# Performance work log

Hardware: AMD Instinct MI355X
Metric: run time of the kernel (lower is better)

Reference implementation:

```python
import jax, jax.numpy as jnp
import numpy as np
from jax import lax


def _l2norm(x):
    # normalize rows: x / ||x||_2, matching torch vector_norm along dim=-1
    return x / jnp.linalg.norm(x, axis=-1, keepdims=True)


def setup_inputs() -> dict:
    key = jax.random.key(0)
    k1, k2, k3, k4, k5 = jax.random.split(key, 5)
    B, N, Ds, Dd = 64, 20000, 4096, 2048
    return {
        "f_content": jax.random.normal(k1, (B, Ds), dtype=jnp.float32),
        "f_distorsion": jax.random.normal(k2, (B, Dd), dtype=jnp.float32),
        "semantic_db": jax.random.normal(k3, (N, Ds), dtype=jnp.float32),
        "distorsion_db": jax.random.normal(k4, (N, Dd), dtype=jnp.float32),
        "metrics": jax.random.uniform(k5, (N,), dtype=jnp.float32),
        "K": 9,
    }


def reference(f_content, f_distorsion, semantic_db, distorsion_db, metrics, K):
    # L2-normalize query features and DB features (DB is normalized at init in torch)
    fc = _l2norm(f_content)            # [B, Ds]
    fd = _l2norm(f_distorsion)         # [B, Dd]
    sem_db = _l2norm(semantic_db)      # [N, Ds]
    dst_db = _l2norm(distorsion_db)    # [N, Dd]

    # full cosine similarity matmuls, then descending top-K (== sort desc + slice K)
    sem_cos = fc @ sem_db.T            # [B, N]
    dst_cos = fd @ dst_db.T            # [B, N]
    _, idx_sem = lax.top_k(sem_cos, K)   # [B, K]
    _, idx_dst = lax.top_k(dst_cos, K)   # [B, K]

    # gather metric values for retrieved neighbors; interleave sem/dst per m
    m_sem = metrics[idx_sem]           # [B, K]
    m_dst = metrics[idx_dst]           # [B, K]
    retrieved = jnp.stack([m_sem, m_dst], axis=-1).reshape(m_sem.shape[0], 2 * K)  # [B, 2K]
    result = retrieved.mean(axis=-1)   # [B]
    return result, retrieved
```

## Files before the change

### kernel.cpp

```cpp
#include <hip/hip_runtime.h>
#include <math.h>


typedef _Float16 half8 __attribute__((ext_vector_type(8)));
typedef float    f32x4 __attribute__((ext_vector_type(4)));

#define NDB   20000
#define NQ    64
#define KSEM  4096
#define KDST  2048
#define KC    2048
#define NSTEP (KC / 64)
#define BN    64
#define NTILE 313
#define K2    16
#define SEG   8
#define SEGSZ (NDB / SEG)

__device__ __forceinline__ void async_cp16(const void* g, void* l) {
    __builtin_amdgcn_global_load_lds(
        (const __attribute__((address_space(1))) void*)g,
        (__attribute__((address_space(3))) void*)l, 16, 0, 0);
}

__global__ __launch_bounds__(256) void qsplit_kernel(
    const float* __restrict__ fc, const float* __restrict__ fd,
    _Float16* __restrict__ apack_sem, _Float16* __restrict__ apack_dst)
{
    const int idx = (int)blockIdx.x * 256 + (int)threadIdx.x;
    const int NSEM8 = NQ * KSEM / 8;
    const float* src; _Float16* dst; int row, g8, K;
    if (idx < NSEM8) { src = fc; dst = apack_sem; K = KSEM; row = idx >> 9; g8 = idx & 511; }
    else { const int j = idx - NSEM8; src = fd; dst = apack_dst; K = KDST; row = j >> 8; g8 = j & 255; }

    const float* p = src + (size_t)row * K + g8 * 8;
    const float4 v0 = ((const float4*)p)[0];
    const float4 v1 = ((const float4*)p)[1];
    const float xs[8] = {v0.x, v0.y, v0.z, v0.w, v1.x, v1.y, v1.z, v1.w};
    half8 hi, lo;
    #pragma unroll
    for (int e = 0; e < 8; ++e) {
        const _Float16 h = (_Float16)xs[e];
        hi[e] = h;
        lo[e] = (_Float16)((xs[e] - (float)h) * 4096.0f);
    }
    const int sec = g8 >> 2, kg = g8 & 3;
    const int u = (row << 2) + (((row >> 1) & 3) ^ kg);
    half8* d8 = (half8*)dst;
    d8[sec * 512 + u]       = hi;
    d8[sec * 512 + 256 + u] = lo;
}

__global__ __launch_bounds__(256, 2) void score_kernel(
    const float* __restrict__ sdb, const float* __restrict__ ddb,
    const _Float16* __restrict__ apack_sem, const _Float16* __restrict__ apack_dst,
    float* __restrict__ semp0, float* __restrict__ semp1, float* __restrict__ dstp,
    float* __restrict__ nsq0, float* __restrict__ nsq1, float* __restrict__ nsqd)
{
    __shared__ __align__(16) _Float16 A_lds[2][8192];
    __shared__ __align__(16) float    B_lds[2][4096];

    const int tid  = threadIdx.x;
    const int lane = tid & 63, w = tid >> 6;
    const int bid  = (int)blockIdx.x;
    const int mkc  = bid / NTILE;
    const int nt   = bid % NTILE;
    const int n0   = nt * BN;

    const float* D; const _Float16* AP; float *SOUT, *NOUT; int Ks, koff;
    if (mkc == 0)      { D=sdb; AP=apack_sem; SOUT=semp0; NOUT=nsq0; Ks=KSEM; koff=0;  }
    else if (mkc == 1) { D=sdb; AP=apack_sem; SOUT=semp1; NOUT=nsq1; Ks=KSEM; koff=KC; }
    else               { D=ddb; AP=apack_dst; SOUT=dstp;  NOUT=nsqd; Ks=KDST; koff=0;  }

    const int u0 = w * 128 + lane,      r0 = u0 >> 3, c0 = (u0 & 7) ^ (r0 & 7);
    const int u1 = u0 + 64,             r1 = u1 >> 3, c1 = (u1 & 7) ^ (r1 & 7);
    const int rg0 = (n0 + r0 < NDB) ? n0 + r0 : NDB - 1;
    const int rg1 = (n0 + r1 < NDB) ? n0 + r1 : NDB - 1;
    const float* gB0 = D + (size_t)rg0 * Ks + koff + c0 * 4;
    const float* gB1 = D + (size_t)rg1 * Ks + koff + c1 * 4;
    const uint4* gA = (const uint4*)AP + ((size_t)koff >> 5) * 512 + w * 64 + lane;

    const int lr = lane & 15, kg = lane >> 4;
    const int qh = w >> 1, nh = w & 1;
    const int rowA0 = qh * 32 + lr;
    const int rowA1 = rowA0 + 16;
    const int uA0 = ((rowA0 << 2) + (((rowA0 >> 1) & 3) ^ kg)) * 8;
    const int uA1 = ((rowA1 << 2) + (((rowA1 >> 1) & 3) ^ kg)) * 8;
    const int rB0 = nh * 32 + lr;
    const int rB1 = rB0 + 16;
    const int oB00 = rB0 * 32 + (((kg * 2 + 0) ^ (rB0 & 7)) << 2);
    const int oB01 = rB0 * 32 + (((kg * 2 + 1) ^ (rB0 & 7)) << 2);
    const int oB10 = rB1 * 32 + (((kg * 2 + 0) ^ (rB1 & 7)) << 2);
    const int oB11 = rB1 * 32 + (((kg * 2 + 1) ^ (rB1 & 7)) << 2);

    f32x4 acc_h[2][2], acc_x[2][2];
    const f32x4 zz = {0.f, 0.f, 0.f, 0.f};
    #pragma unroll
    for (int i = 0; i < 2; ++i)
        #pragma unroll
        for (int j = 0; j < 2; ++j) { acc_h[i][j] = zz; acc_x[i][j] = zz; }
    float sq0 = 0.f, sq1 = 0.f;

    auto STAGE = [&](int s, int buf) {
        #pragma unroll
        for (int sec = 0; sec < 2; ++sec) {
            const size_t gsec = (size_t)(2 * s + sec);
            async_cp16(gA + gsec * 512,       &A_lds[buf][sec * 4096 + w * 512]);
            async_cp16(gA + gsec * 512 + 256, &A_lds[buf][sec * 4096 + 2048 + w * 512]);
            async_cp16(gB0 + gsec * 32, &B_lds[buf][sec * 2048 + w * 512]);
            async_cp16(gB1 + gsec * 32, &B_lds[buf][sec * 2048 + w * 512 + 256]);
        }
    };

    auto COMPUTE = [&](int buf) {
        #pragma unroll
        for (int sec = 0; sec < 2; ++sec) {
            const float*    Bb = &B_lds[buf][sec * 2048];
            const _Float16* Ab = &A_lds[buf][sec * 4096];
            half8 bh0, bl0, bh1, bl1;
            {
                const f32x4 p = *(const f32x4*)(Bb + oB00);
                const f32x4 q = *(const f32x4*)(Bb + oB01);
                const float xs[8] = {p[0], p[1], p[2], p[3], q[0], q[1], q[2], q[3]};
                #pragma unroll
                for (int e = 0; e < 8; ++e) {
                    const float x = xs[e];
                    sq0 = fmaf(x, x, sq0);
                    const _Float16 h = (_Float16)x;
                    bh0[e] = h;
                    bl0[e] = (_Float16)((x - (float)h) * 4096.0f);
                }
            }
            {
                const f32x4 p = *(const f32x4*)(Bb + oB10);
                const f32x4 q = *(const f32x4*)(Bb + oB11);
                const float xs[8] = {p[0], p[1], p[2], p[3], q[0], q[1], q[2], q[3]};
                #pragma unroll
                for (int e = 0; e < 8; ++e) {
                    const float x = xs[e];
                    sq1 = fmaf(x, x, sq1);
                    const _Float16 h = (_Float16)x;
                    bh1[e] = h;
                    bl1[e] = (_Float16)((x - (float)h) * 4096.0f);
                }
            }
            const half8 ah0 = *(const half8*)(Ab + uA0);
            const half8 av0 = *(const half8*)(Ab + 2048 + uA0);
            const half8 ah1 = *(const half8*)(Ab + uA1);
            const half8 av1 = *(const half8*)(Ab + 2048 + uA1);

            acc_h[0][0] = __builtin_amdgcn_mfma_f32_16x16x32_f16(ah0, bh0, acc_h[0][0], 0, 0, 0);
            acc_x[0][0] = __builtin_amdgcn_mfma_f32_16x16x32_f16(ah0, bl0, acc_x[0][0], 0, 0, 0);
            acc_x[0][0] = __builtin_amdgcn_mfma_f32_16x16x32_f16(av0, bh0, acc_x[0][0], 0, 0, 0);
            acc_h[0][1] = __builtin_amdgcn_mfma_f32_16x16x32_f16(ah0, bh1, acc_h[0][1], 0, 0, 0);
            acc_x[0][1] = __builtin_amdgcn_mfma_f32_16x16x32_f16(ah0, bl1, acc_x[0][1], 0, 0, 0);
            acc_x[0][1] = __builtin_amdgcn_mfma_f32_16x16x32_f16(av0, bh1, acc_x[0][1], 0, 0, 0);
            acc_h[1][0] = __builtin_amdgcn_mfma_f32_16x16x32_f16(ah1, bh0, acc_h[1][0], 0, 0, 0);
            acc_x[1][0] = __builtin_amdgcn_mfma_f32_16x16x32_f16(ah1, bl0, acc_x[1][0], 0, 0, 0);
            acc_x[1][0] = __builtin_amdgcn_mfma_f32_16x16x32_f16(av1, bh0, acc_x[1][0], 0, 0, 0);
            acc_h[1][1] = __builtin_amdgcn_mfma_f32_16x16x32_f16(ah1, bh1, acc_h[1][1], 0, 0, 0);
            acc_x[1][1] = __builtin_amdgcn_mfma_f32_16x16x32_f16(ah1, bl1, acc_x[1][1], 0, 0, 0);
            acc_x[1][1] = __builtin_amdgcn_mfma_f32_16x16x32_f16(av1, bh1, acc_x[1][1], 0, 0, 0);
        }
    };

    STAGE(0, 0); STAGE(1, 1);

    for (int s = 0; s < NSTEP; ++s) {
        if (s < NSTEP - 1) { asm volatile("s_waitcnt vmcnt(8)" ::: "memory"); }
        else               { asm volatile("s_waitcnt vmcnt(0)" ::: "memory"); }
        __builtin_amdgcn_s_barrier();
        COMPUTE(s & 1);
        __builtin_amdgcn_s_barrier();
        if (s + 2 < NSTEP) STAGE(s + 2, s & 1);
    }

    sq0 += __shfl_xor(sq0, 16); sq0 += __shfl_xor(sq0, 32);
    sq1 += __shfl_xor(sq1, 16); sq1 += __shfl_xor(sq1, 32);
    if (qh == 0 && lane < 16) {
        const int nn0 = n0 + nh * 32 + lane;
        const int nn1 = nn0 + 16;
        if (nn0 < NDB) NOUT[nn0] = sq0;
        if (nn1 < NDB) NOUT[nn1] = sq1;
    }

    #pragma unroll
    for (int i = 0; i < 2; ++i)
        #pragma unroll
        for (int j = 0; j < 2; ++j) {
            const int n = n0 + nh * 32 + j * 16 + lr;
            if (n < NDB) {
                #pragma unroll
                for (int rr = 0; rr < 4; ++rr) {
                    const int q = qh * 32 + i * 16 + kg * 4 + rr;
                    SOUT[(size_t)q * NDB + n] = acc_h[i][j][rr] + acc_x[i][j][rr] * (1.0f / 4096.0f);
                }
            }
        }
}

__global__ __launch_bounds__(256) void topk_seg_kernel(
    const float* __restrict__ semp0, const float* __restrict__ semp1,
    const float* __restrict__ dstp,
    const float* __restrict__ nsq0, const float* __restrict__ nsq1,
    const float* __restrict__ nsqd,
    float* __restrict__ cand_val, int* __restrict__ cand_idx)
{
    __shared__ float sv[256][K2];
    __shared__ int   si[256][K2];

    const int tid = threadIdx.x;
    const int mb  = (int)blockIdx.x >> 3;
    const int seg = (int)blockIdx.x & 7;
    const int b = mb & 63;
    const int m = mb >> 6;

    float v[K2]; int ix[K2];
    #pragma unroll
    for (int k = 0; k < K2; ++k) { v[k] = -INFINITY; ix[k] = 0x7fffffff; }

    const size_t roff = (size_t)b * NDB;
    const int iend = (seg + 1) * SEGSZ;
    for (int i = seg * SEGSZ + tid; i < iend; i += 256) {
        float sval;
        if (m == 0) {
            sval = (semp0[roff + i] + semp1[roff + i]) * (1.0f / sqrtf(nsq0[i] + nsq1[i]));
        } else {
            sval = dstp[roff + i] * (1.0f / sqrtf(nsqd[i]));
        }
        if (sval > v[0]) {
            bool bt[K2];
            bt[0] = true;
            #pragma unroll
            for (int j = 1; j < K2; ++j) bt[j] = sval > v[j];
            #pragma unroll
            for (int j = 0; j < K2 - 1; ++j) {
                v[j]  = bt[j+1] ? v[j+1]  : (bt[j] ? sval : v[j]);
                ix[j] = bt[j+1] ? ix[j+1] : (bt[j] ? i    : ix[j]);
            }
            v[K2-1]  = bt[K2-1] ? sval : v[K2-1];
            ix[K2-1] = bt[K2-1] ? i    : ix[K2-1];
        }
    }

    #pragma unroll
    for (int k = 0; k < K2; ++k) { sv[tid][k] = v[k]; si[tid][k] = ix[k]; }
    __syncthreads();

    for (int s2 = 128; s2 >= 1; s2 >>= 1) {
        if (tid < s2) {
            float rv[K2]; int ri[K2];
            int pa = K2 - 1, pb = K2 - 1;
            #pragma unroll
            for (int k = K2 - 1; k >= 0; --k) {
                const float va = sv[tid][pa];      const int ia = si[tid][pa];
                const float vb = sv[tid + s2][pb]; const int ib = si[tid + s2][pb];
                const bool takeA = (va > vb) || (va == vb && ia < ib);
                rv[k] = takeA ? va : vb;
                ri[k] = takeA ? ia : ib;
                if (takeA) --pa; else --pb;
            }
            #pragma unroll
            for (int k = 0; k < K2; ++k) { sv[tid][k] = rv[k]; si[tid][k] = ri[k]; }
        }
        __syncthreads();
    }

    if (tid < K2) {
        cand_val[(size_t)mb * 128 + seg * K2 + tid] = sv[0][K2 - 1 - tid];
        cand_idx[(size_t)mb * 128 + seg * K2 + tid] = si[0][K2 - 1 - tid];
    }
}

__global__ __launch_bounds__(128) void merge_kernel(
    const float* __restrict__ cand_val, const int* __restrict__ cand_idx,
    const float* __restrict__ metrics, float* __restrict__ out_ret)
{
    __shared__ float v[128];
    __shared__ int   id[128];
    const int tid = threadIdx.x;
    const int mb  = (int)blockIdx.x;
    const int b = mb & 63;
    const int m = mb >> 6;
    v[tid]  = cand_val[(size_t)mb * 128 + tid];
    id[tid] = cand_idx[(size_t)mb * 128 + tid];
    __syncthreads();
    const float mv = v[tid];
    const int   mi = id[tid];
    int rank = 0;
    for (int j = 0; j < 128; ++j)
        rank += (v[j] > mv) || (v[j] == mv && id[j] < mi);
    if (rank < 9) out_ret[(size_t)b * 18 + 2 * rank + m] = metrics[mi];
}

__global__ void finalize_kernel(float* __restrict__ d_out)
{
    const int b = threadIdx.x;
    const float* r = d_out + 64 + (size_t)b * 18;
    float s = 0.f;
    #pragma unroll
    for (int j = 0; j < 18; ++j) s += r[j];
    d_out[b] = s * (1.0f / 18.0f);
}

extern "C" void kernel_launch(void* const* d_in, const int* in_sizes, int n_in,
                              void* d_out, int out_size, void* d_ws, size_t ws_size,
                              hipStream_t stream)
{
    const float* fc  = (const float*)d_in[0];
    const float* fd  = (const float*)d_in[1];
    const float* sdb = (const float*)d_in[2];
    const float* ddb = (const float*)d_in[3];
    const float* met = (const float*)d_in[4];

    float* semp0 = (float*)d_ws;
    float* semp1 = semp0 + (size_t)NQ * NDB;
    float* dstp  = semp1 + (size_t)NQ * NDB;
    float* nsq0  = dstp  + (size_t)NQ * NDB;
    float* nsq1  = nsq0 + NDB;
    float* nsqd  = nsq1 + NDB;
    _Float16* apack_sem = (_Float16*)(nsqd + NDB);
    _Float16* apack_dst = apack_sem + (size_t)NQ * KSEM * 2;
    float* cand_val = (float*)(apack_dst + (size_t)NQ * KDST * 2);
    int*   cand_idx = (int*)(cand_val + 128 * 128);

    float* out = (float*)d_out;

    qsplit_kernel<<<dim3(192), dim3(256), 0, stream>>>(fc, fd, apack_sem, apack_dst);
    score_kernel<<<dim3(3 * NTILE), dim3(256), 0, stream>>>(
        sdb, ddb, apack_sem, apack_dst, semp0, semp1, dstp, nsq0, nsq1, nsqd);
    topk_seg_kernel<<<dim3(128 * SEG), dim3(256), 0, stream>>>(
        semp0, semp1, dstp, nsq0, nsq1, nsqd, cand_val, cand_idx);
    merge_kernel<<<dim3(128), dim3(128), 0, stream>>>(cand_val, cand_idx, met, out + 64);
    finalize_kernel<<<dim3(1), dim3(64), 0, stream>>>(out);
}
```

Baseline: 169.6 us.

## Drop query low-part MFMAs and add exact FP32 rerank of top-16 candidates

The query side now keeps only the fp16 high part, which removes one third of the MFMAs and halves the A-tile LDS footprint and loads. Occupancy is raised to 3 blocks per SM. To make up for the lower-precision scores, the merge kernel keeps the top 16 candidates, and a new rerank kernel recomputes their exact fp32 cosine similarity before choosing the top 9. This adds a small extra kernel, and the final answer can be wrong if a true top-9 item falls outside the approximate top-16.

```diff
diff --git a/kernel.cpp b/kernel.cpp
--- a/kernel.cpp
+++ b/kernel.cpp
@@ -37,27 +37,21 @@
     const float4 v0 = ((const float4*)p)[0];
     const float4 v1 = ((const float4*)p)[1];
     const float xs[8] = {v0.x, v0.y, v0.z, v0.w, v1.x, v1.y, v1.z, v1.w};
-    half8 hi, lo;
-    #pragma unroll
-    for (int e = 0; e < 8; ++e) {
-        const _Float16 h = (_Float16)xs[e];
-        hi[e] = h;
-        lo[e] = (_Float16)((xs[e] - (float)h) * 4096.0f);
-    }
+    half8 hi;
+    #pragma unroll
+    for (int e = 0; e < 8; ++e) hi[e] = (_Float16)xs[e];
     const int sec = g8 >> 2, kg = g8 & 3;
     const int u = (row << 2) + (((row >> 1) & 3) ^ kg);
-    half8* d8 = (half8*)dst;
-    d8[sec * 512 + u]       = hi;
-    d8[sec * 512 + 256 + u] = lo;
-}
-
-__global__ __launch_bounds__(256, 2) void score_kernel(
+    ((half8*)dst)[sec * 256 + u] = hi;
+}
+
+__global__ __launch_bounds__(256, 3) void score_kernel(
     const float* __restrict__ sdb, const float* __restrict__ ddb,
     const _Float16* __restrict__ apack_sem, const _Float16* __restrict__ apack_dst,
     float* __restrict__ semp0, float* __restrict__ semp1, float* __restrict__ dstp,
     float* __restrict__ nsq0, float* __restrict__ nsq1, float* __restrict__ nsqd)
 {
-    __shared__ __align__(16) _Float16 A_lds[2][8192];
+    __shared__ __align__(16) _Float16 A_lds[2][4096];
     __shared__ __align__(16) float    B_lds[2][4096];
 
     const int tid  = threadIdx.x;
@@ -78,7 +72,7 @@
     const int rg1 = (n0 + r1 < NDB) ? n0 + r1 : NDB - 1;
     const float* gB0 = D + (size_t)rg0 * Ks + koff + c0 * 4;
     const float* gB1 = D + (size_t)rg1 * Ks + koff + c1 * 4;
-    const uint4* gA = (const uint4*)AP + ((size_t)koff >> 5) * 512 + w * 64 + lane;
+    const uint4* gA = (const uint4*)AP + ((size_t)koff >> 5) * 256 + w * 64 + lane;
 
     const int lr = lane & 15, kg = lane >> 4;
     const int qh = w >> 1, nh = w & 1;
@@ -105,10 +99,9 @@
         #pragma unroll
         for (int sec = 0; sec < 2; ++sec) {
             const size_t gsec = (size_t)(2 * s + sec);
-            async_cp16(gA + gsec * 512,       &A_lds[buf][sec * 4096 + w * 512]);
-            async_cp16(gA + gsec * 512 + 256, &A_lds[buf][sec * 4096 + 2048 + w * 512]);
-            async_cp16(gB0 + gsec * 32, &B_lds[buf][sec * 2048 + w * 512]);
-            async_cp16(gB1 + gsec * 32, &B_lds[buf][sec * 2048 + w * 512 + 256]);
+            async_cp16(gA + gsec * 256,  &A_lds[buf][sec * 2048 + w * 512]);
+            async_cp16(gB0 + gsec * 32,  &B_lds[buf][sec * 2048 + w * 512]);
+            async_cp16(gB1 + gsec * 32,  &B_lds[buf][sec * 2048 + w * 512 + 256]);
         }
     };
 
@@ -116,7 +109,7 @@
         #pragma unroll
         for (int sec = 0; sec < 2; ++sec) {
             const float*    Bb = &B_lds[buf][sec * 2048];
-            const _Float16* Ab = &A_lds[buf][sec * 4096];
+            const _Float16* Ab = &A_lds[buf][sec * 2048];
             half8 bh0, bl0, bh1, bl1;
             {
                 const f32x4 p = *(const f32x4*)(Bb + oB00);
@@ -145,29 +138,23 @@
                 }
             }
             const half8 ah0 = *(const half8*)(Ab + uA0);
-            const half8 av0 = *(const half8*)(Ab + 2048 + uA0);
             const half8 ah1 = *(const half8*)(Ab + uA1);
-            const half8 av1 = *(const half8*)(Ab + 2048 + uA1);
 
             acc_h[0][0] = __builtin_amdgcn_mfma_f32_16x16x32_f16(ah0, bh0, acc_h[0][0], 0, 0, 0);
             acc_x[0][0] = __builtin_amdgcn_mfma_f32_16x16x32_f16(ah0, bl0, acc_x[0][0], 0, 0, 0);
-            acc_x[0][0] = __builtin_amdgcn_mfma_f32_16x16x32_f16(av0, bh0, acc_x[0][0], 0, 0, 0);
             acc_h[0][1] = __builtin_amdgcn_mfma_f32_16x16x32_f16(ah0, bh1, acc_h[0][1], 0, 0, 0);
             acc_x[0][1] = __builtin_amdgcn_mfma_f32_16x16x32_f16(ah0, bl1, acc_x[0][1], 0, 0, 0);
-            acc_x[0][1] = __builtin_amdgcn_mfma_f32_16x16x32_f16(av0, bh1, acc_x[0][1], 0, 0, 0);
             acc_h[1][0] = __builtin_amdgcn_mfma_f32_16x16x32_f16(ah1, bh0, acc_h[1][0], 0, 0, 0);
             acc_x[1][0] = __builtin_amdgcn_mfma_f32_16x16x32_f16(ah1, bl0, acc_x[1][0], 0, 0, 0);
-            acc_x[1][0] = __builtin_amdgcn_mfma_f32_16x16x32_f16(av1, bh0, acc_x[1][0], 0, 0, 0);
             acc_h[1][1] = __builtin_amdgcn_mfma_f32_16x16x32_f16(ah1, bh1, acc_h[1][1], 0, 0, 0);
             acc_x[1][1] = __builtin_amdgcn_mfma_f32_16x16x32_f16(ah1, bl1, acc_x[1][1], 0, 0, 0);
-            acc_x[1][1] = __builtin_amdgcn_mfma_f32_16x16x32_f16(av1, bh1, acc_x[1][1], 0, 0, 0);
         }
     };
 
     STAGE(0, 0); STAGE(1, 1);
 
     for (int s = 0; s < NSTEP; ++s) {
-        if (s < NSTEP - 1) { asm volatile("s_waitcnt vmcnt(8)" ::: "memory"); }
+        if (s < NSTEP - 1) { asm volatile("s_waitcnt vmcnt(6)" ::: "memory"); }
         else               { asm volatile("s_waitcnt vmcnt(0)" ::: "memory"); }
         __builtin_amdgcn_s_barrier();
         COMPUTE(s & 1);
@@ -274,14 +261,12 @@
 
 __global__ __launch_bounds__(128) void merge_kernel(
     const float* __restrict__ cand_val, const int* __restrict__ cand_idx,
-    const float* __restrict__ metrics, float* __restrict__ out_ret)
+    int* __restrict__ idx_ws)
 {
     __shared__ float v[128];
     __shared__ int   id[128];
     const int tid = threadIdx.x;
     const int mb  = (int)blockIdx.x;
-    const int b = mb & 63;
-    const int m = mb >> 6;
     v[tid]  = cand_val[(size_t)mb * 128 + tid];
     id[tid] = cand_idx[(size_t)mb * 128 + tid];
     __syncthreads();
@@ -290,7 +275,63 @@
     int rank = 0;
     for (int j = 0; j < 128; ++j)
         rank += (v[j] > mv) || (v[j] == mv && id[j] < mi);
-    if (rank < 9) out_ret[(size_t)b * 18 + 2 * rank + m] = metrics[mi];
+    if (rank < K2) idx_ws[(size_t)mb * K2 + rank] = mi;
+}
+
+__global__ __launch_bounds__(256) void rerank_kernel(
+    const float* __restrict__ fc, const float* __restrict__ fd,
+    const float* __restrict__ sdb, const float* __restrict__ ddb,
+    const int* __restrict__ idx_ws, const float* __restrict__ metrics,
+    float* __restrict__ out_ret)
+{
+    __shared__ float cosv[K2];
+    __shared__ int   cidx[K2];
+
+    const int tid = threadIdx.x;
+    const int lane = tid & 63, w = tid >> 6;
+    const int bid = (int)blockIdx.x;
+    const int b = bid & 63;
+    const int m = bid >> 6;
+
+    const float* Q  = (m == 0) ? fc + (size_t)b * KSEM : fd + (size_t)b * KDST;
+    const float* DB = (m == 0) ? sdb : ddb;
+    const int Ks = (m == 0) ? KSEM : KDST;
+    const int nf4 = Ks / 4;
+
+    for (int c = w; c < K2; c += 4) {
+        const int idx = idx_ws[(size_t)bid * K2 + c];
+        const float4* Q4 = (const float4*)Q;
+        const float4* R4 = (const float4*)(DB + (size_t)idx * Ks);
+        float dot = 0.f, sq = 0.f;
+        for (int it = lane; it < nf4; it += 64) {
+            const float4 qv = Q4[it];
+            const float4 rv = R4[it];
+            dot = fmaf(qv.x, rv.x, dot); sq = fmaf(rv.x, rv.x, sq);
+            dot = fmaf(qv.y, rv.y, dot); sq = fmaf(rv.y, rv.y, sq);
+            dot = fmaf(qv.z, rv.z, dot); sq = fmaf(rv.z, rv.z, sq);
+            dot = fmaf(qv.w, rv.w, dot); sq = fmaf(rv.w, rv.w, sq);
+        }
+        #pragma unroll
+        for (int off = 1; off < 64; off <<= 1) {
+            dot += __shfl_xor(dot, off);
+            sq  += __shfl_xor(sq,  off);
+        }
+        if (lane == 0) {
+            cosv[c] = dot / sqrtf(sq);
+            cidx[c] = idx;
+        }
+    }
+    __syncthreads();
+
+    if (tid < K2) {
+        const float v = cosv[tid];
+        const int   id = cidx[tid];
+        int rank = 0;
+        #pragma unroll
+        for (int j = 0; j < K2; ++j)
+            rank += (cosv[j] > v) || (cosv[j] == v && cidx[j] < id);
+        if (rank < 9) out_ret[(size_t)b * 18 + 2 * rank + m] = metrics[id];
+    }
 }
 
 __global__ void finalize_kernel(float* __restrict__ d_out)
@@ -320,9 +361,10 @@
     float* nsq1  = nsq0 + NDB;
     float* nsqd  = nsq1 + NDB;
     _Float16* apack_sem = (_Float16*)(nsqd + NDB);
-    _Float16* apack_dst = apack_sem + (size_t)NQ * KSEM * 2;
-    float* cand_val = (float*)(apack_dst + (size_t)NQ * KDST * 2);
+    _Float16* apack_dst = apack_sem + (size_t)NQ * KSEM;
+    float* cand_val = (float*)(apack_dst + (size_t)NQ * KDST);
     int*   cand_idx = (int*)(cand_val + 128 * 128);
+    int*   idx_ws   = cand_idx + 128 * 128;
 
     float* out = (float*)d_out;
 
@@ -331,6 +373,8 @@
         sdb, ddb, apack_sem, apack_dst, semp0, semp1, dstp, nsq0, nsq1, nsqd);
     topk_seg_kernel<<<dim3(128 * SEG), dim3(256), 0, stream>>>(
         semp0, semp1, dstp, nsq0, nsq1, nsqd, cand_val, cand_idx);
-    merge_kernel<<<dim3(128), dim3(128), 0, stream>>>(cand_val, cand_idx, met, out + 64);
+    merge_kernel<<<dim3(128), dim3(128), 0, stream>>>(cand_val, cand_idx, idx_ws);
+    rerank_kernel<<<dim3(128), dim3(256), 0, stream>>>(
+        fc, fd, sdb, ddb, idx_ws, met, out + 64);
     finalize_kernel<<<dim3(1), dim3(64), 0, stream>>>(out);
 }
```

Result: slower. 216.9 us (+27.9%).

## Double score-kernel N tile to 128 rows with 32-wide K steps

Applied to the files above, without the earlier changes.

Changes the score kernel tile from 64 DB rows by 64 K per step to 128 DB rows by 32 K per step, halving the number of blocks. Each wave now computes a 32x64 output sub-tile with 4 B fragments, so each A fragment loaded from LDS is reused across more MFMAs and the query matrix is re-read from global memory half as often. The async-copy staging, the waitcnt depth and the epilogue indexing are reworked to match. The cost is more accumulator registers per thread, fewer blocks (which may lower occupancy and load balance across CUs), and more barrier iterations per block because each step is shorter.

```diff
diff --git a/kernel.cpp b/kernel.cpp
--- a/kernel.cpp
+++ b/kernel.cpp
@@ -10,9 +10,9 @@
 #define KSEM  4096
 #define KDST  2048
 #define KC    2048
-#define NSTEP (KC / 64)
-#define BN    64
-#define NTILE 313
+#define NSTEP (KC / 32)
+#define BN    128
+#define NTILE 157
 #define K2    16
 #define SEG   8
 #define SEGSZ (NDB / SEG)
@@ -57,7 +57,7 @@
     float* __restrict__ semp0, float* __restrict__ semp1, float* __restrict__ dstp,
     float* __restrict__ nsq0, float* __restrict__ nsq1, float* __restrict__ nsqd)
 {
-    __shared__ __align__(16) _Float16 A_lds[2][8192];
+    __shared__ __align__(16) _Float16 A_lds[2][4096];
     __shared__ __align__(16) float    B_lds[2][4096];
 
     const int tid  = threadIdx.x;
@@ -72,12 +72,15 @@
     else if (mkc == 1) { D=sdb; AP=apack_sem; SOUT=semp1; NOUT=nsq1; Ks=KSEM; koff=KC; }
     else               { D=ddb; AP=apack_dst; SOUT=dstp;  NOUT=nsqd; Ks=KDST; koff=0;  }
 
-    const int u0 = w * 128 + lane,      r0 = u0 >> 3, c0 = (u0 & 7) ^ (r0 & 7);
-    const int u1 = u0 + 64,             r1 = u1 >> 3, c1 = (u1 & 7) ^ (r1 & 7);
-    const int rg0 = (n0 + r0 < NDB) ? n0 + r0 : NDB - 1;
-    const int rg1 = (n0 + r1 < NDB) ? n0 + r1 : NDB - 1;
-    const float* gB0 = D + (size_t)rg0 * Ks + koff + c0 * 4;
-    const float* gB1 = D + (size_t)rg1 * Ks + koff + c1 * 4;
+    const float* gBp[4];
+    #pragma unroll
+    for (int k2 = 0; k2 < 4; ++k2) {
+        const int u = w * 256 + k2 * 64 + lane;
+        const int r = u >> 3;
+        const int c = (u & 7) ^ (r & 7);
+        const int rg = (n0 + r < NDB) ? n0 + r : NDB - 1;
+        gBp[k2] = D + (size_t)rg * Ks + koff + c * 4;
+    }
     const uint4* gA = (const uint4*)AP + ((size_t)koff >> 5) * 512 + w * 64 + lane;
 
     const int lr = lane & 15, kg = lane >> 4;
@@ -86,88 +89,67 @@
     const int rowA1 = rowA0 + 16;
     const int uA0 = ((rowA0 << 2) + (((rowA0 >> 1) & 3) ^ kg)) * 8;
     const int uA1 = ((rowA1 << 2) + (((rowA1 >> 1) & 3) ^ kg)) * 8;
-    const int rB0 = nh * 32 + lr;
-    const int rB1 = rB0 + 16;
-    const int oB00 = rB0 * 32 + (((kg * 2 + 0) ^ (rB0 & 7)) << 2);
-    const int oB01 = rB0 * 32 + (((kg * 2 + 1) ^ (rB0 & 7)) << 2);
-    const int oB10 = rB1 * 32 + (((kg * 2 + 0) ^ (rB1 & 7)) << 2);
-    const int oB11 = rB1 * 32 + (((kg * 2 + 1) ^ (rB1 & 7)) << 2);
-
-    f32x4 acc_h[2][2], acc_x[2][2];
+    int oB0[4], oB1[4];
+    #pragma unroll
+    for (int j = 0; j < 4; ++j) {
+        const int rB = nh * 64 + j * 16 + lr;
+        oB0[j] = rB * 32 + (((kg * 2 + 0) ^ (rB & 7)) << 2);
+        oB1[j] = rB * 32 + (((kg * 2 + 1) ^ (rB & 7)) << 2);
+    }
+
+    f32x4 acc_h[2][4], acc_x[2][4];
     const f32x4 zz = {0.f, 0.f, 0.f, 0.f};
     #pragma unroll
     for (int i = 0; i < 2; ++i)
         #pragma unroll
-        for (int j = 0; j < 2; ++j) { acc_h[i][j] = zz; acc_x[i][j] = zz; }
-    float sq0 = 0.f, sq1 = 0.f;
+        for (int j = 0; j < 4; ++j) { acc_h[i][j] = zz; acc_x[i][j] = zz; }
+    float sq[4] = {0.f, 0.f, 0.f, 0.f};
 
     auto STAGE = [&](int s, int buf) {
-        #pragma unroll
-        for (int sec = 0; sec < 2; ++sec) {
-            const size_t gsec = (size_t)(2 * s + sec);
-            async_cp16(gA + gsec * 512,       &A_lds[buf][sec * 4096 + w * 512]);
-            async_cp16(gA + gsec * 512 + 256, &A_lds[buf][sec * 4096 + 2048 + w * 512]);
-            async_cp16(gB0 + gsec * 32, &B_lds[buf][sec * 2048 + w * 512]);
-            async_cp16(gB1 + gsec * 32, &B_lds[buf][sec * 2048 + w * 512 + 256]);
-        }
+        async_cp16(gA + (size_t)s * 512,       &A_lds[buf][w * 512]);
+        async_cp16(gA + (size_t)s * 512 + 256, &A_lds[buf][2048 + w * 512]);
+        #pragma unroll
+        for (int k2 = 0; k2 < 4; ++k2)
+            async_cp16(gBp[k2] + (size_t)s * 32, &B_lds[buf][w * 1024 + k2 * 256]);
     };
 
     auto COMPUTE = [&](int buf) {
-        #pragma unroll
-        for (int sec = 0; sec < 2; ++sec) {
-            const float*    Bb = &B_lds[buf][sec * 2048];
-            const _Float16* Ab = &A_lds[buf][sec * 4096];
-            half8 bh0, bl0, bh1, bl1;
-            {
-                const f32x4 p = *(const f32x4*)(Bb + oB00);
-                const f32x4 q = *(const f32x4*)(Bb + oB01);
-                const float xs[8] = {p[0], p[1], p[2], p[3], q[0], q[1], q[2], q[3]};
-                #pragma unroll
-                for (int e = 0; e < 8; ++e) {
-                    const float x = xs[e];
-                    sq0 = fmaf(x, x, sq0);
-                    const _Float16 h = (_Float16)x;
-                    bh0[e] = h;
-                    bl0[e] = (_Float16)((x - (float)h) * 4096.0f);
-                }
+        const float*    Bb = &B_lds[buf][0];
+        const _Float16* Ab = &A_lds[buf][0];
+        half8 bh[4], bl[4];
+        #pragma unroll
+        for (int j = 0; j < 4; ++j) {
+            const f32x4 p = *(const f32x4*)(Bb + oB0[j]);
+            const f32x4 q = *(const f32x4*)(Bb + oB1[j]);
+            const float xs[8] = {p[0], p[1], p[2], p[3], q[0], q[1], q[2], q[3]};
+            #pragma unroll
+            for (int e = 0; e < 8; ++e) {
+                const float x = xs[e];
+                sq[j] = fmaf(x, x, sq[j]);
+                const _Float16 h = (_Float16)x;
+                bh[j][e] = h;
+                bl[j][e] = (_Float16)((x - (float)h) * 4096.0f);
             }
-            {
-                const f32x4 p = *(const f32x4*)(Bb + oB10);
-                const f32x4 q = *(const f32x4*)(Bb + oB11);
-                const float xs[8] = {p[0], p[1], p[2], p[3], q[0], q[1], q[2], q[3]};
-                #pragma unroll
-                for (int e = 0; e < 8; ++e) {
-                    const float x = xs[e];
-                    sq1 = fmaf(x, x, sq1);
-                    const _Float16 h = (_Float16)x;
-                    bh1[e] = h;
-                    bl1[e] = (_Float16)((x - (float)h) * 4096.0f);
-                }
-            }
-            const half8 ah0 = *(const half8*)(Ab + uA0);
-            const half8 av0 = *(const half8*)(Ab + 2048 + uA0);
-            const half8 ah1 = *(const half8*)(Ab + uA1);
-            const half8 av1 = *(const half8*)(Ab + 2048 + uA1);
-
-            acc_h[0][0] = __builtin_amdgcn_mfma_f32_16x16x32_f16(ah0, bh0, acc_h[0][0], 0, 0, 0);
-            acc_x[0][0] = __builtin_amdgcn_mfma_f32_16x16x32_f16(ah0, bl0, acc_x[0][0], 0, 0, 0);
-            acc_x[0][0] = __builtin_amdgcn_mfma_f32_16x16x32_f16(av0, bh0, acc_x[0][0], 0, 0, 0);
-            acc_h[0][1] = __builtin_amdgcn_mfma_f32_16x16x32_f16(ah0, bh1, acc_h[0][1], 0, 0, 0);
-            acc_x[0][1] = __builtin_amdgcn_mfma_f32_16x16x32_f16(ah0, bl1, acc_x[0][1], 0, 0, 0);
-            acc_x[0][1] = __builtin_amdgcn_mfma_f32_16x16x32_f16(av0, bh1, acc_x[0][1], 0, 0, 0);
-            acc_h[1][0] = __builtin_amdgcn_mfma_f32_16x16x32_f16(ah1, bh0, acc_h[1][0], 0, 0, 0);
-            acc_x[1][0] = __builtin_amdgcn_mfma_f32_16x16x32_f16(ah1, bl0, acc_x[1][0], 0, 0, 0);
-            acc_x[1][0] = __builtin_amdgcn_mfma_f32_16x16x32_f16(av1, bh0, acc_x[1][0], 0, 0, 0);
-            acc_h[1][1] = __builtin_amdgcn_mfma_f32_16x16x32_f16(ah1, bh1, acc_h[1][1], 0, 0, 0);
-            acc_x[1][1] = __builtin_amdgcn_mfma_f32_16x16x32_f16(ah1, bl1, acc_x[1][1], 0, 0, 0);
-            acc_x[1][1] = __builtin_amdgcn_mfma_f32_16x16x32_f16(av1, bh1, acc_x[1][1], 0, 0, 0);
+        }
+        const half8 ah0 = *(const half8*)(Ab + uA0);
+        const half8 av0 = *(const half8*)(Ab + 2048 + uA0);
+        const half8 ah1 = *(const half8*)(Ab + uA1);
+        const half8 av1 = *(const half8*)(Ab + 2048 + uA1);
+        #pragma unroll
+        for (int j = 0; j < 4; ++j) {
+            acc_h[0][j] = __builtin_amdgcn_mfma_f32_16x16x32_f16(ah0, bh[j], acc_h[0][j], 0, 0, 0);
+            acc_x[0][j] = __builtin_amdgcn_mfma_f32_16x16x32_f16(ah0, bl[j], acc_x[0][j], 0, 0, 0);
+            acc_x[0][j] = __builtin_amdgcn_mfma_f32_16x16x32_f16(av0, bh[j], acc_x[0][j], 0, 0, 0);
+            acc_h[1][j] = __builtin_amdgcn_mfma_f32_16x16x32_f16(ah1, bh[j], acc_h[1][j], 0, 0, 0);
+            acc_x[1][j] = __builtin_amdgcn_mfma_f32_16x16x32_f16(ah1, bl[j], acc_x[1][j], 0, 0, 0);
+            acc_x[1][j] = __builtin_amdgcn_mfma_f32_16x16x32_f16(av1, bh[j], acc_x[1][j], 0, 0, 0);
         }
     };
 
     STAGE(0, 0); STAGE(1, 1);
 
     for (int s = 0; s < NSTEP; ++s) {
-        if (s < NSTEP - 1) { asm volatile("s_waitcnt vmcnt(8)" ::: "memory"); }
+        if (s < NSTEP - 1) { asm volatile("s_waitcnt vmcnt(6)" ::: "memory"); }
         else               { asm volatile("s_waitcnt vmcnt(0)" ::: "memory"); }
         __builtin_amdgcn_s_barrier();
         COMPUTE(s & 1);
@@ -175,20 +157,24 @@
         if (s + 2 < NSTEP) STAGE(s + 2, s & 1);
     }
 
-    sq0 += __shfl_xor(sq0, 16); sq0 += __shfl_xor(sq0, 32);
-    sq1 += __shfl_xor(sq1, 16); sq1 += __shfl_xor(sq1, 32);
+    #pragma unroll
+    for (int j = 0; j < 4; ++j) {
+        sq[j] += __shfl_xor(sq[j], 16);
+        sq[j] += __shfl_xor(sq[j], 32);
+    }
     if (qh == 0 && lane < 16) {
-        const int nn0 = n0 + nh * 32 + lane;
-        const int nn1 = nn0 + 16;
-        if (nn0 < NDB) NOUT[nn0] = sq0;
-        if (nn1 < NDB) NOUT[nn1] = sq1;
+        #pragma unroll
+        for (int j = 0; j < 4; ++j) {
+            const int nn = n0 + nh * 64 + j * 16 + lane;
+            if (nn < NDB) NOUT[nn] = sq[j];
+        }
     }
 
     #pragma unroll
     for (int i = 0; i < 2; ++i)
         #pragma unroll
-        for (int j = 0; j < 2; ++j) {
-            const int n = n0 + nh * 32 + j * 16 + lr;
+        for (int j = 0; j < 4; ++j) {
+            const int n = n0 + nh * 64 + j * 16 + lr;
             if (n < NDB) {
                 #pragma unroll
                 for (int rr = 0; rr < 4; ++rr) {
```

Measured after the change: 161.2 us (median of 2 runs). 1.05x faster.
